# Performance work log

Hardware: AMD Instinct MI355X
Metric: run time of the kernel (lower is better)

Reference implementation:

```python
import jax, jax.numpy as jnp
import numpy as np

B, L, D, H = 2, 2048, 1024, 16
d = D // H  # head dim = 64


def setup_inputs() -> dict:
    key = jax.random.key(0)
    ks = jax.random.split(key, 6)
    X = jax.random.normal(ks[0], (B, L, D), dtype=jnp.float32)
    scale = 0.02
    Wq = scale * jax.random.normal(ks[1], (D, D), dtype=jnp.float32)
    Wk = scale * jax.random.normal(ks[2], (D, D), dtype=jnp.float32)
    Wv = scale * jax.random.normal(ks[3], (D, D), dtype=jnp.float32)
    Wc = scale * jax.random.normal(ks[4], (D, D), dtype=jnp.float32)
    Ltri = scale * jax.random.normal(ks[5], (H, d, d), dtype=jnp.float32)
    return {"X": X, "Wq": Wq, "Wk": Wk, "Wv": Wv, "Wc": Wc, "Ltri": Ltri}


def reference(X, Wq, Wk, Wv, Wc, Ltri):
    # torch nn.Linear: y = x @ W.T (bias=False); dropout is identity in eval.
    Bsz, Lq, Dm = X.shape
    Q = (X @ Wq.T).reshape(Bsz, Lq, H, d)
    K = (X @ Wk.T).reshape(Bsz, Lq, H, d)
    V = (X @ Wv.T).reshape(Bsz, Lq, H, d)
    # Causal linear attention: cumulative sum of per-position K outer V.
    # W[b,l,h,:,:] = sum_{t<=l} K[b,t,h,:] outer V[b,t,h,:]
    KV = jnp.einsum('blhd,blhe->blhde', K, V)  # [B,L,H,d,d]
    KVc = jnp.cumsum(KV, axis=1)
    Y = jnp.einsum('blhd,blhde->blhe', Q, KVc)  # [B,L,H,d]
    # Learned SPD head-mixing matrix Bm = Lm @ Lm.T with Lm lower-triangular.
    mask = jnp.tril(jnp.ones((1, d, d), dtype=X.dtype))
    Lm = Ltri * mask  # [H,d,d]
    Bm = Lm @ jnp.swapaxes(Lm, -2, -1)  # [H,d,d]
    Y = jnp.einsum('hed,blhd->blhe', Bm, Y)
    Y = Y.reshape(Bsz, Lq, Dm)
    return Y @ Wc.T
```

## Files before the change

### kernel.cpp

```cpp
#include <hip/hip_runtime.h>


#define DEV static __device__ __forceinline__

typedef unsigned short u16;
typedef unsigned long long u64;
typedef __attribute__((ext_vector_type(4))) float f32x4;
typedef __attribute__((ext_vector_type(8))) short bf16x8;

DEV u16 f2bf(float f){
  union { float f; unsigned u; } v; v.f = f;
  unsigned r = v.u + 0x7FFFu + ((v.u >> 16) & 1u);
  return (u16)(r >> 16);
}

DEV void store_val(float* p, float v){ *p = v; }
DEV void store_val(u16* p, float v){ *p = f2bf(v); }

DEV void gload16(const void* g, void* l){
  __builtin_amdgcn_global_load_lds((const __attribute__((address_space(1))) void*)g,
                                   (__attribute__((address_space(3))) void*)l, 16, 0, 0);
}

__global__ __launch_bounds__(256) void prep_kernel(
    const float* __restrict__ X, u16* __restrict__ Xb,
    const float* __restrict__ Wq, u16* __restrict__ Wqb,
    const float* __restrict__ Wk, u16* __restrict__ Wkb,
    const float* __restrict__ Wv, u16* __restrict__ Wvb,
    const float* __restrict__ Wc, u16* __restrict__ Wcb,
    const float* __restrict__ Ltri, u16* __restrict__ Bmb)
{
  const int bx = blockIdx.x, tid = threadIdx.x;
  if(bx < 16){
    __shared__ float Lm[64][65];
    int h = bx;
    const float* src = Ltri + (size_t)h * 4096;
    for(int i = tid; i < 4096; i += 256){
      int e = i >> 6, k = i & 63;
      Lm[e][k] = (k <= e) ? src[i] : 0.f;
    }
    __syncthreads();
    u16* out = Bmb + (size_t)h * 4096;
    for(int i = tid; i < 4096; i += 256){
      int e = i >> 6, dk = i & 63;
      float sum = 0.f;
      int kmax = e < dk ? e : dk;
      for(int k = 0; k <= kmax; k++) sum += Lm[e][k] * Lm[dk][k];
      out[i] = f2bf(sum);
    }
  } else {
    const int n0 = 4194304, n1 = 1048576, n2 = 1048576, n3 = 1048576, n4 = 1048576;
    int total = (n0 + n1 + n2 + n3 + n4) >> 2;
    for(int i = (bx - 16) * 256 + tid; i < total; i += 2048 * 256){
      int e = i << 2;
      const float* s; u16* d;
      if(e < n0){ s = X + e; d = Xb + e; }
      else if(e < n0 + n1){ s = Wq + (e - n0); d = Wqb + (e - n0); }
      else if(e < n0 + n1 + n2){ s = Wk + (e - n0 - n1); d = Wkb + (e - n0 - n1); }
      else if(e < n0 + n1 + n2 + n3){ s = Wv + (e - n0 - n1 - n2); d = Wvb + (e - n0 - n1 - n2); }
      else { s = Wc + (e - n0 - n1 - n2 - n3); d = Wcb + (e - n0 - n1 - n2 - n3); }
      float4 v = *(const float4*)s;
      u64 pk = (u64)f2bf(v.x) | ((u64)f2bf(v.y) << 16) | ((u64)f2bf(v.z) << 32) | ((u64)f2bf(v.w) << 48);
      *(u64*)d = pk;
    }
  }
}

template<typename OutT>
DEV void gemm128_p2(const u16* __restrict__ A, const u16* __restrict__ W,
                    OutT* __restrict__ C, int bx, int by, int N, int K)
{
  __shared__ u16 L[3][8192];
  const int tid = threadIdx.x;
  const int wid = tid >> 6, lane = tid & 63;
  const int wr = wid >> 1, wc = wid & 1;
  const int lr = lane & 15, lq = lane >> 4;
  const u16* Ag = A + (size_t)(bx * 128) * K;
  const u16* Wg = W + (size_t)(by * 128) * K;

  const int p0 = tid >> 3, p1 = 32 + (tid >> 3);
  const int cl0 = (tid & 7) ^ (p0 & 7);
  const int cl1 = (tid & 7) ^ (p1 & 7);
  const int srow0 = 2 * p0 + (cl0 >> 2), skc0 = (cl0 & 3) * 8;
  const int srow1 = 2 * p1 + (cl1 >> 2), skc1 = (cl1 & 3) * 8;

  auto stagef = [&](int kt, int buf){
    gload16(Ag + (size_t)srow0 * K + kt * 32 + skc0, &L[buf][tid * 8]);
    gload16(Ag + (size_t)srow1 * K + kt * 32 + skc1, &L[buf][2048 + tid * 8]);
    gload16(Wg + (size_t)srow0 * K + kt * 32 + skc0, &L[buf][4096 + tid * 8]);
    gload16(Wg + (size_t)srow1 * K + kt * 32 + skc1, &L[buf][6144 + tid * 8]);
  };

  const int nt = K >> 5;
  f32x4 acc[4][4] = {};
  stagef(0, 0);
  stagef(1, 1);
  int cur = 0;
  for(int t = 0; t < nt; t++){
    if(t < nt - 1) asm volatile("s_waitcnt vmcnt(4)" ::: "memory");
    else           asm volatile("s_waitcnt vmcnt(0)" ::: "memory");
    __builtin_amdgcn_s_barrier();
    __builtin_amdgcn_sched_barrier(0);
    if(t + 2 < nt){
      int n2 = cur >= 1 ? cur - 1 : cur + 2;
      stagef(t + 2, n2);
    }
    const u16* Lb = L[cur];
    bf16x8 af[4], bfr[4];
#pragma unroll
    for(int i = 0; i < 4; i++){
      int row = wr * 64 + i * 16 + lr;
      int rh = row >> 1;
      int cph = (lq | ((row & 1) << 2)) ^ (rh & 7);
      af[i] = *(const bf16x8*)&Lb[rh * 64 + cph * 8];
    }
#pragma unroll
    for(int j = 0; j < 4; j++){
      int row = wc * 64 + j * 16 + lr;
      int rh = row >> 1;
      int cph = (lq | ((row & 1) << 2)) ^ (rh & 7);
      bfr[j] = *(const bf16x8*)&Lb[4096 + rh * 64 + cph * 8];
    }
#pragma unroll
    for(int i = 0; i < 4; i++)
#pragma unroll
      for(int j = 0; j < 4; j++)
        acc[i][j] = __builtin_amdgcn_mfma_f32_16x16x32_bf16(af[i], bfr[j], acc[i][j], 0, 0, 0);
    cur = cur == 2 ? 0 : cur + 1;
  }
#pragma unroll
  for(int i = 0; i < 4; i++)
#pragma unroll
    for(int j = 0; j < 4; j++)
#pragma unroll
      for(int r = 0; r < 4; r++){
        int row = bx * 128 + wr * 64 + i * 16 + (lane >> 4) * 4 + r;
        int col = by * 128 + wc * 64 + j * 16 + lr;
        store_val(C + (size_t)row * N + col, acc[i][j][r]);
      }
}

template<typename OutT>
DEV void gemm128_p3(const u16* __restrict__ A, const u16* __restrict__ W,
                    OutT* __restrict__ C, int bx, int by, int N, int K)
{
  __shared__ u16 L[4][8192];
  const int tid = threadIdx.x;
  const int wid = tid >> 6, lane = tid & 63;
  const int wr = wid >> 1, wc = wid & 1;
  const int lr = lane & 15, lq = lane >> 4;
  const u16* Ag = A + (size_t)(bx * 128) * K;
  const u16* Wg = W + (size_t)(by * 128) * K;

  const int p0 = tid >> 3, p1 = 32 + (tid >> 3);
  const int cl0 = (tid & 7) ^ (p0 & 7);
  const int cl1 = (tid & 7) ^ (p1 & 7);
  const int srow0 = 2 * p0 + (cl0 >> 2), skc0 = (cl0 & 3) * 8;
  const int srow1 = 2 * p1 + (cl1 >> 2), skc1 = (cl1 & 3) * 8;

  auto stagef = [&](int kt, int buf){
    gload16(Ag + (size_t)srow0 * K + kt * 32 + skc0, &L[buf][tid * 8]);
    gload16(Ag + (size_t)srow1 * K + kt * 32 + skc1, &L[buf][2048 + tid * 8]);
    gload16(Wg + (size_t)srow0 * K + kt * 32 + skc0, &L[buf][4096 + tid * 8]);
    gload16(Wg + (size_t)srow1 * K + kt * 32 + skc1, &L[buf][6144 + tid * 8]);
  };

  const int nt = K >> 5;
  f32x4 acc[4][4] = {};
  stagef(0, 0);
  stagef(1, 1);
  stagef(2, 2);
  for(int t = 0; t < nt; t++){
    if(t < nt - 2)       asm volatile("s_waitcnt vmcnt(8)" ::: "memory");
    else if(t == nt - 2) asm volatile("s_waitcnt vmcnt(4)" ::: "memory");
    else                 asm volatile("s_waitcnt vmcnt(0)" ::: "memory");
    __builtin_amdgcn_s_barrier();
    __builtin_amdgcn_sched_barrier(0);
    if(t + 3 < nt) stagef(t + 3, (t + 3) & 3);
    const u16* Lb = L[t & 3];
    bf16x8 af[4], bfr[4];
#pragma unroll
    for(int i = 0; i < 4; i++){
      int row = wr * 64 + i * 16 + lr;
      int rh = row >> 1;
      int cph = (lq | ((row & 1) << 2)) ^ (rh & 7);
      af[i] = *(const bf16x8*)&Lb[rh * 64 + cph * 8];
    }
#pragma unroll
    for(int j = 0; j < 4; j++){
      int row = wc * 64 + j * 16 + lr;
      int rh = row >> 1;
      int cph = (lq | ((row & 1) << 2)) ^ (rh & 7);
      bfr[j] = *(const bf16x8*)&Lb[4096 + rh * 64 + cph * 8];
    }
#pragma unroll
    for(int i = 0; i < 4; i++)
#pragma unroll
      for(int j = 0; j < 4; j++)
        acc[i][j] = __builtin_amdgcn_mfma_f32_16x16x32_bf16(af[i], bfr[j], acc[i][j], 0, 0, 0);
  }
#pragma unroll
  for(int i = 0; i < 4; i++)
#pragma unroll
    for(int j = 0; j < 4; j++)
#pragma unroll
      for(int r = 0; r < 4; r++){
        int row = bx * 128 + wr * 64 + i * 16 + (lane >> 4) * 4 + r;
        int col = by * 128 + wc * 64 + j * 16 + lr;
        store_val(C + (size_t)row * N + col, acc[i][j][r]);
      }
}

__global__ __launch_bounds__(256) void qkv_gemm(
    const u16* __restrict__ Xb,
    const u16* __restrict__ Wq, const u16* __restrict__ Wk, const u16* __restrict__ Wv,
    u16* __restrict__ Q, u16* __restrict__ Ko, u16* __restrict__ V,
    const u16* __restrict__ Wcb, const u16* __restrict__ Bmb, u16* __restrict__ Wcpb)
{
  if(blockIdx.y >= 24){
    int rt = blockIdx.x & 7, h = (blockIdx.x >> 3) + ((blockIdx.y - 24) << 2);
    int wid = threadIdx.x >> 6, lane = threadIdx.x & 63;
    int lr = lane & 15, lk8 = (lane >> 4) * 8, lq = lane >> 4;
    const u16* ab  = Wcb + (size_t)(rt * 128) * 1024 + h * 64;
    const u16* bm  = Bmb + (size_t)h * 4096;
    f32x4 acc[2][4] = {};
#pragma unroll
    for(int i = 0; i < 2; i++){
      int mf = wid * 2 + i;
#pragma unroll
      for(int ks = 0; ks < 2; ks++){
        bf16x8 a = *(const bf16x8*)(ab + (size_t)(mf * 16 + lr) * 1024 + ks * 32 + lk8);
#pragma unroll
        for(int nf = 0; nf < 4; nf++){
          bf16x8 bfr = *(const bf16x8*)(bm + (nf * 16 + lr) * 64 + ks * 32 + lk8);
          acc[i][nf] = __builtin_amdgcn_mfma_f32_16x16x32_bf16(a, bfr, acc[i][nf], 0, 0, 0);
        }
      }
    }
#pragma unroll
    for(int i = 0; i < 2; i++)
#pragma unroll
      for(int nf = 0; nf < 4; nf++)
#pragma unroll
        for(int r = 0; r < 4; r++){
          int row = rt * 128 + (wid * 2 + i) * 16 + lq * 4 + r;
          int col = h * 64 + nf * 16 + lr;
          Wcpb[(size_t)row * 1024 + col] = f2bf(acc[i][nf][r]);
        }
    return;
  }
  int sel = blockIdx.y >> 3, byl = blockIdx.y & 7;
  const u16* W = sel == 0 ? Wq : sel == 1 ? Wk : Wv;
  u16* C = sel == 0 ? Q : sel == 1 ? Ko : V;
  gemm128_p2<u16>(Xb, W, C, blockIdx.x, byl, 1024, 1024);
}

__global__ __launch_bounds__(256) void out_gemm(
    const u16* __restrict__ Yb, const u16* __restrict__ Wcpb, float* __restrict__ out)
{
  gemm128_p3<float>(Yb, Wcpb, out, blockIdx.x, blockIdx.y, 1024, 1024);
}

__global__ __launch_bounds__(256) void state_chunk(
    const u16* __restrict__ Kb, const u16* __restrict__ Vb,
    u16* __restrict__ VT, float* __restrict__ Sc)
{
  int bh = blockIdx.x, c = blockIdx.y;
  int b = bh >> 4, h = bh & 15;
  int tid = threadIdx.x;
  __shared__ u16 Kt[128][72];
  __shared__ u16 Vt[128][72];
  __shared__ u16 KtT[64][136];
  __shared__ u16 VtT[64][136];
  int rr = tid >> 3;
  int cc = (tid & 7) * 8;
  const u16* kg = Kb + (size_t)(b * 2048 + c * 128) * 1024 + h * 64;
  const u16* vg = Vb + (size_t)(b * 2048 + c * 128) * 1024 + h * 64;
#pragma unroll
  for(int p = 0; p < 4; p++){
    int row = rr + p * 32;
    *(int4*)&Kt[row][cc] = *(const int4*)(kg + (size_t)row * 1024 + cc);
    *(int4*)&Vt[row][cc] = *(const int4*)(vg + (size_t)row * 1024 + cc);
  }
  __syncthreads();
  int d = tid >> 2, tseg = (tid & 3) * 32;
#pragma unroll
  for(int j = 0; j < 32; j += 8){
    u16 tk[8] __attribute__((aligned(16)));
    u16 tv[8] __attribute__((aligned(16)));
#pragma unroll
    for(int q = 0; q < 8; q++){
      tk[q] = Kt[tseg + j + q][d];
      tv[q] = Vt[tseg + j + q][d];
    }
    *(int4*)&KtT[d][tseg + j] = *(const int4*)tk;
    *(int4*)&VtT[d][tseg + j] = *(const int4*)tv;
  }
  __syncthreads();
  {
    u16* vto = VT + (size_t)bh * 64 * 2048 + (size_t)d * 2048 + c * 128 + tseg;
#pragma unroll
    for(int j = 0; j < 32; j += 8)
      *(int4*)(vto + j) = *(const int4*)&VtT[d][tseg + j];
  }
  int wid = tid >> 6, lane = tid & 63;
  int wr = wid >> 1, wc = wid & 1;
  int lr = lane & 15, lk8 = (lane >> 4) * 8, lq = lane >> 4;
  f32x4 acc[2][2] = {};
#pragma unroll
  for(int ks = 0; ks < 4; ks++){
    bf16x8 a[2], bb[2];
#pragma unroll
    for(int i = 0; i < 2; i++) a[i]  = *(const bf16x8*)&VtT[wr * 32 + i * 16 + lr][ks * 32 + lk8];
#pragma unroll
    for(int j = 0; j < 2; j++) bb[j] = *(const bf16x8*)&KtT[wc * 32 + j * 16 + lr][ks * 32 + lk8];
#pragma unroll
    for(int i = 0; i < 2; i++)
#pragma unroll
      for(int j = 0; j < 2; j++)
        acc[i][j] = __builtin_amdgcn_mfma_f32_16x16x32_bf16(a[i], bb[j], acc[i][j], 0, 0, 0);
  }
  float* out = Sc + ((size_t)bh * 16 + c) * 4096;
#pragma unroll
  for(int i = 0; i < 2; i++)
#pragma unroll
    for(int j = 0; j < 2; j++)
#pragma unroll
      for(int r = 0; r < 4; r++){
        int e = wr * 32 + i * 16 + lq * 4 + r, dk = wc * 32 + j * 16 + lr;
        out[e * 64 + dk] = acc[i][j][r];
      }
}

__global__ __launch_bounds__(256) void prefix_state(const float* __restrict__ Sc, u16* __restrict__ Scb)
{
  int bh = blockIdx.x >> 2, part = blockIdx.x & 3;
  int e4 = part * 256 + threadIdx.x;
  const float4* s = (const float4*)(Sc + (size_t)bh * 65536) + e4;
  u16* d = Scb + (size_t)bh * 65536 + e4 * 4;
  float4 run = {0.f, 0.f, 0.f, 0.f};
  for(int c = 0; c < 16; c++){
    float4 v = s[(size_t)c * 1024];
    u64 pk = (u64)f2bf(run.x) | ((u64)f2bf(run.y) << 16) | ((u64)f2bf(run.z) << 32) | ((u64)f2bf(run.w) << 48);
    *(u64*)(d + (size_t)c * 4096) = pk;
    run.x += v.x; run.y += v.y; run.z += v.z; run.w += v.w;
  }
}

__global__ __launch_bounds__(256) void chunk_attn(
    const u16* __restrict__ Q, const u16* __restrict__ Kmat,
    const u16* __restrict__ VT, const u16* __restrict__ Scb, u16* __restrict__ Y)
{
  int bh = blockIdx.x, c = blockIdx.y;
  int b = bh >> 4, h = bh & 15;
  int t = threadIdx.x, wid = t >> 6, lane = t & 63;
  int lr = lane & 15, lk8 = (lane >> 4) * 8, lq = lane >> 4;
  __shared__ u16 S[128 * 128];
  const u16* qg = Q    + (size_t)(b * 2048 + c * 128) * 1024 + h * 64;
  const u16* kg = Kmat + (size_t)(b * 2048 + c * 128) * 1024 + h * 64;
  const u16* scb = Scb + ((size_t)bh * 16 + c) * 4096;
  const u16* vt  = VT + (size_t)bh * 64 * 2048 + (size_t)c * 128;
  u16* yg = Y + (size_t)(b * 2048 + c * 128) * 1024 + h * 64;

  bf16x8 a[2][2];
#pragma unroll
  for(int mi = 0; mi < 2; mi++){
    int mf = wid + mi * 4;
    int Rm = mf * 16;
    if((mf & 1) == 0){
      int zr = Rm + (lane >> 2), zc = Rm + 16 + (lane & 3) * 4;
      int zoff = ((zr * 128 + zc) * 2) ^ ((zr & 7) << 4);
      *(u64*)((char*)S + zoff) = 0ULL;
    }
#pragma unroll
    for(int ks = 0; ks < 2; ks++) a[mi][ks] = *(const bf16x8*)(qg + (size_t)(Rm + lr) * 1024 + ks * 32 + lk8);
    for(int nf = 0; nf <= mf; nf++){
      f32x4 acc = {};
#pragma unroll
      for(int ks = 0; ks < 2; ks++){
        bf16x8 bb = *(const bf16x8*)(kg + (size_t)(nf * 16 + lr) * 1024 + ks * 32 + lk8);
        acc = __builtin_amdgcn_mfma_f32_16x16x32_bf16(a[mi][ks], bb, acc, 0, 0, 0);
      }
#pragma unroll
      for(int r = 0; r < 4; r++){
        int row = lq * 4 + r, col = lr;
        float v = acc[r];
        if(nf == mf && col > row) v = 0.f;
        int grow = Rm + row, gcol = nf * 16 + col;
        int off = ((grow * 128 + gcol) * 2) ^ ((grow & 7) << 4);
        *(u16*)((char*)S + off) = f2bf(v);
      }
    }
  }
  f32x4 acc2[2][4] = {};
#pragma unroll
  for(int nf = 0; nf < 4; nf++)
#pragma unroll
    for(int ks = 0; ks < 2; ks++){
      bf16x8 bb = *(const bf16x8*)(scb + (nf * 16 + lr) * 64 + ks * 32 + lk8);
#pragma unroll
      for(int mi = 0; mi < 2; mi++)
        acc2[mi][nf] = __builtin_amdgcn_mfma_f32_16x16x32_bf16(a[mi][ks], bb, acc2[mi][nf], 0, 0, 0);
    }
  int ks0 = wid >> 1;
  int row0 = wid * 16 + lr;
  int row1 = (wid + 4) * 16 + lr;
  for(int ks = 0; ks <= ks0 + 2; ks++){
    bf16x8 bb[4];
#pragma unroll
    for(int nf = 0; nf < 4; nf++)
      bb[nf] = *(const bf16x8*)(vt + (size_t)(nf * 16 + lr) * 2048 + ks * 32 + lk8);
    if(ks <= ks0){
      int off = ((row0 * 128 + ks * 32 + lk8) * 2) ^ ((row0 & 7) << 4);
      bf16x8 af = *(const bf16x8*)((char*)S + off);
#pragma unroll
      for(int nf = 0; nf < 4; nf++)
        acc2[0][nf] = __builtin_amdgcn_mfma_f32_16x16x32_bf16(af, bb[nf], acc2[0][nf], 0, 0, 0);
    }
    {
      int off = ((row1 * 128 + ks * 32 + lk8) * 2) ^ ((row1 & 7) << 4);
      bf16x8 af = *(const bf16x8*)((char*)S + off);
#pragma unroll
      for(int nf = 0; nf < 4; nf++)
        acc2[1][nf] = __builtin_amdgcn_mfma_f32_16x16x32_bf16(af, bb[nf], acc2[1][nf], 0, 0, 0);
    }
  }
#pragma unroll
  for(int mi = 0; mi < 2; mi++){
    int Rm = (wid + mi * 4) * 16;
#pragma unroll
    for(int nf = 0; nf < 4; nf++)
#pragma unroll
      for(int r = 0; r < 4; r++){
        int grow = Rm + lq * 4 + r, gcol = nf * 16 + lr;
        yg[(size_t)grow * 1024 + gcol] = f2bf(acc2[mi][nf][r]);
      }
  }
}

extern "C" void kernel_launch(void* const* d_in, const int* in_sizes, int n_in,
                              void* d_out, int out_size, void* d_ws, size_t ws_size,
                              hipStream_t stream)
{
  const float* X    = (const float*)d_in[0];
  const float* Wq   = (const float*)d_in[1];
  const float* Wk   = (const float*)d_in[2];
  const float* Wv   = (const float*)d_in[3];
  const float* Wc   = (const float*)d_in[4];
  const float* Ltri = (const float*)d_in[5];
  float* out = (float*)d_out;

  char* ws = (char*)d_ws;
  size_t off = 0;
  auto carve = [&](size_t bytes) -> char* {
    char* p = ws + off;
    off += (bytes + 255) & ~(size_t)255;
    return p;
  };
  u16* Xb   = (u16*)carve((size_t)4194304 * 2);
  u16* Wqb  = (u16*)carve((size_t)1048576 * 2);
  u16* Wkb  = (u16*)carve((size_t)1048576 * 2);
  u16* Wvb  = (u16*)carve((size_t)1048576 * 2);
  u16* Wcb  = (u16*)carve((size_t)1048576 * 2);
  u16* Wcpb = (u16*)carve((size_t)1048576 * 2);
  u16* Bmb  = (u16*)carve((size_t)65536 * 2);
  u16* Qb   = (u16*)carve((size_t)4194304 * 2);
  u16* Kb   = (u16*)carve((size_t)4194304 * 2);
  u16* Vb   = (u16*)carve((size_t)4194304 * 2);
  u16* VT   = (u16*)carve((size_t)4194304 * 2);
  float* Sc = (float*)carve((size_t)2097152 * 4);
  u16* Scb  = (u16*)carve((size_t)2097152 * 2);
  u16* Yb   = (u16*)carve((size_t)4194304 * 2);
  (void)in_sizes; (void)n_in; (void)out_size; (void)ws_size;

  prep_kernel<<<2064, 256, 0, stream>>>(X, Xb, Wq, Wqb, Wk, Wkb, Wv, Wvb, Wc, Wcb, Ltri, Bmb);
  qkv_gemm<<<dim3(32, 28), 256, 0, stream>>>(Xb, Wqb, Wkb, Wvb, Qb, Kb, Vb, Wcb, Bmb, Wcpb);
  state_chunk<<<dim3(32, 16), 256, 0, stream>>>(Kb, Vb, VT, Sc);
  prefix_state<<<128, 256, 0, stream>>>(Sc, Scb);
  chunk_attn<<<dim3(32, 16), 256, 0, stream>>>(Qb, Kb, VT, Scb, Yb);
  out_gemm<<<dim3(32, 8), 256, 0, stream>>>(Yb, Wcpb, out);
}
```

Measured before the change: 106.0 us.

## Fuse chunk state and prefix-scan via last-block atomic counter, move Wc·Bm fold

Merges the per-chunk state kernel and the prefix-sum kernel into one launch. The last block to finish for each (batch, head) runs the prefix scan, detected with an atomic counter that qkv_gemm zeroes. The Wc·Bm weight-fold blocks move from the QKV GEMM grid into this fused kernel, which shortens the QKV grid and removes one launch and its gap. The cost is a serialized scan tail in one block per head and correctness that depends on threadfence ordering and the counter reset.

Result: slower. 144.1 us (+35.9%).

```diff
diff --git a/kernel.cpp b/kernel.cpp
--- a/kernel.cpp
+++ b/kernel.cpp
@@ -134,7 +134,7 @@
     for(int j = 0; j < 4; j++)
 #pragma unroll
       for(int r = 0; r < 4; r++){
-        int row = bx * 128 + wr * 64 + i * 16 + (lane >> 4) * 4 + r;
+        int row = bx * 128 + wr * 64 + i * 16 + lq * 4 + r;
         int col = by * 128 + wc * 64 + j * 16 + lr;
         store_val(C + (size_t)row * N + col, acc[i][j][r]);
       }
@@ -205,7 +205,7 @@
     for(int j = 0; j < 4; j++)
 #pragma unroll
       for(int r = 0; r < 4; r++){
-        int row = bx * 128 + wr * 64 + i * 16 + (lane >> 4) * 4 + r;
+        int row = bx * 128 + wr * 64 + i * 16 + lq * 4 + r;
         int col = by * 128 + wc * 64 + j * 16 + lr;
         store_val(C + (size_t)row * N + col, acc[i][j][r]);
       }
@@ -215,11 +215,32 @@
     const u16* __restrict__ Xb,
     const u16* __restrict__ Wq, const u16* __restrict__ Wk, const u16* __restrict__ Wv,
     u16* __restrict__ Q, u16* __restrict__ Ko, u16* __restrict__ V,
-    const u16* __restrict__ Wcb, const u16* __restrict__ Bmb, u16* __restrict__ Wcpb)
-{
-  if(blockIdx.y >= 24){
-    int rt = blockIdx.x & 7, h = (blockIdx.x >> 3) + ((blockIdx.y - 24) << 2);
-    int wid = threadIdx.x >> 6, lane = threadIdx.x & 63;
+    unsigned* __restrict__ ctr)
+{
+  if(blockIdx.x == 0 && blockIdx.y == 0 && threadIdx.x < 32) ctr[threadIdx.x] = 0u;
+  int sel = blockIdx.y >> 3, byl = blockIdx.y & 7;
+  const u16* W = sel == 0 ? Wq : sel == 1 ? Wk : Wv;
+  u16* C = sel == 0 ? Q : sel == 1 ? Ko : V;
+  gemm128_p2<u16>(Xb, W, C, blockIdx.x, byl, 1024, 1024);
+}
+
+__global__ __launch_bounds__(256) void out_gemm(
+    const u16* __restrict__ Yb, const u16* __restrict__ Wcpb, float* __restrict__ out)
+{
+  gemm128_p3<float>(Yb, Wcpb, out, blockIdx.x, blockIdx.y, 1024, 1024);
+}
+
+__global__ __launch_bounds__(256) void state_pf(
+    const u16* __restrict__ Kb, const u16* __restrict__ Vb,
+    u16* __restrict__ VT, float* __restrict__ Sc, u16* __restrict__ Scb,
+    const u16* __restrict__ Wcb, const u16* __restrict__ Bmb, u16* __restrict__ Wcpb,
+    unsigned* __restrict__ ctr)
+{
+  const int bxg = blockIdx.x, tid = threadIdx.x;
+  if(bxg >= 512){
+    int ob = bxg - 512;
+    int rt = ob & 7, h = ob >> 3;
+    int wid = tid >> 6, lane = tid & 63;
     int lr = lane & 15, lk8 = (lane >> 4) * 8, lq = lane >> 4;
     const u16* ab  = Wcb + (size_t)(rt * 128) * 1024 + h * 64;
     const u16* bm  = Bmb + (size_t)h * 4096;
@@ -249,29 +270,14 @@
         }
     return;
   }
-  int sel = blockIdx.y >> 3, byl = blockIdx.y & 7;
-  const u16* W = sel == 0 ? Wq : sel == 1 ? Wk : Wv;
-  u16* C = sel == 0 ? Q : sel == 1 ? Ko : V;
-  gemm128_p2<u16>(Xb, W, C, blockIdx.x, byl, 1024, 1024);
-}
-
-__global__ __launch_bounds__(256) void out_gemm(
-    const u16* __restrict__ Yb, const u16* __restrict__ Wcpb, float* __restrict__ out)
-{
-  gemm128_p3<float>(Yb, Wcpb, out, blockIdx.x, blockIdx.y, 1024, 1024);
-}
-
-__global__ __launch_bounds__(256) void state_chunk(
-    const u16* __restrict__ Kb, const u16* __restrict__ Vb,
-    u16* __restrict__ VT, float* __restrict__ Sc)
-{
-  int bh = blockIdx.x, c = blockIdx.y;
+
+  int bh = bxg >> 4, c = bxg & 15;
   int b = bh >> 4, h = bh & 15;
-  int tid = threadIdx.x;
   __shared__ u16 Kt[128][72];
   __shared__ u16 Vt[128][72];
   __shared__ u16 KtT[64][136];
   __shared__ u16 VtT[64][136];
+  __shared__ int sflag;
   int rr = tid >> 3;
   int cc = (tid & 7) * 8;
   const u16* kg = Kb + (size_t)(b * 2048 + c * 128) * 1024 + h * 64;
@@ -320,7 +326,7 @@
       for(int j = 0; j < 2; j++)
         acc[i][j] = __builtin_amdgcn_mfma_f32_16x16x32_bf16(a[i], bb[j], acc[i][j], 0, 0, 0);
   }
-  float* out = Sc + ((size_t)bh * 16 + c) * 4096;
+  float* outp = Sc + ((size_t)bh * 16 + c) * 4096;
 #pragma unroll
   for(int i = 0; i < 2; i++)
 #pragma unroll
@@ -328,22 +334,33 @@
 #pragma unroll
       for(int r = 0; r < 4; r++){
         int e = wr * 32 + i * 16 + lq * 4 + r, dk = wc * 32 + j * 16 + lr;
-        out[e * 64 + dk] = acc[i][j][r];
-      }
-}
-
-__global__ __launch_bounds__(256) void prefix_state(const float* __restrict__ Sc, u16* __restrict__ Scb)
-{
-  int bh = blockIdx.x >> 2, part = blockIdx.x & 3;
-  int e4 = part * 256 + threadIdx.x;
-  const float4* s = (const float4*)(Sc + (size_t)bh * 65536) + e4;
-  u16* d = Scb + (size_t)bh * 65536 + e4 * 4;
-  float4 run = {0.f, 0.f, 0.f, 0.f};
-  for(int c = 0; c < 16; c++){
-    float4 v = s[(size_t)c * 1024];
-    u64 pk = (u64)f2bf(run.x) | ((u64)f2bf(run.y) << 16) | ((u64)f2bf(run.z) << 32) | ((u64)f2bf(run.w) << 48);
-    *(u64*)(d + (size_t)c * 4096) = pk;
-    run.x += v.x; run.y += v.y; run.z += v.z; run.w += v.w;
+        outp[e * 64 + dk] = acc[i][j][r];
+      }
+
+  __syncthreads();
+  if(tid == 0){
+    __threadfence();
+    unsigned old = atomicAdd(&ctr[bh], 1u);
+    sflag = (old == 15u);
+  }
+  __syncthreads();
+  if(sflag){
+    __threadfence();
+    const float* sb = Sc + (size_t)bh * 65536;
+    u16* db = Scb + (size_t)bh * 65536;
+#pragma unroll
+    for(int p = 0; p < 4; p++){
+      int e4 = p * 256 + tid;
+      const float4* s = (const float4*)sb + e4;
+      u16* dp = db + e4 * 4;
+      float4 run = {0.f, 0.f, 0.f, 0.f};
+      for(int c2 = 0; c2 < 16; c2++){
+        float4 v = s[(size_t)c2 * 1024];
+        u64 pk = (u64)f2bf(run.x) | ((u64)f2bf(run.y) << 16) | ((u64)f2bf(run.z) << 32) | ((u64)f2bf(run.w) << 48);
+        *(u64*)(dp + (size_t)c2 * 4096) = pk;
+        run.x += v.x; run.y += v.y; run.z += v.z; run.w += v.w;
+      }
+    }
   }
 }
 
@@ -471,12 +488,12 @@
   float* Sc = (float*)carve((size_t)2097152 * 4);
   u16* Scb  = (u16*)carve((size_t)2097152 * 2);
   u16* Yb   = (u16*)carve((size_t)4194304 * 2);
+  unsigned* ctr = (unsigned*)carve(128);
   (void)in_sizes; (void)n_in; (void)out_size; (void)ws_size;
 
   prep_kernel<<<2064, 256, 0, stream>>>(X, Xb, Wq, Wqb, Wk, Wkb, Wv, Wvb, Wc, Wcb, Ltri, Bmb);
-  qkv_gemm<<<dim3(32, 28), 256, 0, stream>>>(Xb, Wqb, Wkb, Wvb, Qb, Kb, Vb, Wcb, Bmb, Wcpb);
-  state_chunk<<<dim3(32, 16), 256, 0, stream>>>(Kb, Vb, VT, Sc);
-  prefix_state<<<128, 256, 0, stream>>>(Sc, Scb);
+  qkv_gemm<<<dim3(32, 24), 256, 0, stream>>>(Xb, Wqb, Wkb, Wvb, Qb, Kb, Vb, ctr);
+  state_pf<<<640, 256, 0, stream>>>(Kb, Vb, VT, Sc, Scb, Wcb, Bmb, Wcpb, ctr);
   chunk_attn<<<dim3(32, 16), 256, 0, stream>>>(Qb, Kb, VT, Scb, Yb);
   out_gemm<<<dim3(32, 8), 256, 0, stream>>>(Yb, Wcpb, out);
 }
```
